# Performance work log

Hardware: AMD Instinct MI355X
Metric: run time of the kernel (lower is better)

Reference implementation:

```python
import jax, jax.numpy as jnp
import numpy as np

V = 50000        # output_size (vocab)
H = 1024         # internal hidden = hidden_size*2
L = 400          # max_length (encoder length)
B = 64
OOV_PAD = 500


def setup_inputs() -> dict:
    key = jax.random.key(0)
    ks = jax.random.split(key, 16)
    s = 0.02
    inp = {
        "input_ids": jax.random.randint(ks[0], (B,), 0, V),
        "hidden": jax.random.normal(ks[1], (1, B, H), jnp.float32),
        "encoder_outputs": jax.random.normal(ks[2], (L, B, H), jnp.float32),
        "full_input": jax.random.randint(ks[3], (B, L), 0, V),
        # parameters
        "emb": jax.random.normal(ks[4], (V, H), jnp.float32) * s,
        "attn_W": jax.random.normal(ks[5], (L, 2 * H), jnp.float32) * s,
        "attn_b": jnp.zeros((L,), jnp.float32),
        "comb_W": jax.random.normal(ks[6], (H, 2 * H), jnp.float32) * s,
        "comb_b": jnp.zeros((H,), jnp.float32),
        "W_ih": jax.random.normal(ks[7], (3 * H, H), jnp.float32) * s,
        "W_hh": jax.random.normal(ks[8], (3 * H, H), jnp.float32) * s,
        "b_ih": jnp.zeros((3 * H,), jnp.float32),
        "b_hh": jnp.zeros((3 * H,), jnp.float32),
        "out_W": jax.random.normal(ks[9], (V, H), jnp.float32) * s,
        "out_b": jnp.zeros((V,), jnp.float32),
        "gen_W": jax.random.normal(ks[10], (1, 2 * H), jnp.float32) * s,
        "gen_b": jnp.zeros((1,), jnp.float32),
    }
    return inp


def _decoder_step(input_ids, hidden, encoder_outputs, full_input,
                  emb, attn_W, attn_b, comb_W, comb_b,
                  W_ih, W_hh, b_ih, b_hh, out_W, out_b, gen_W, gen_b):
    embedded = emb[input_ids]                      # [B,H] (dropout is eval-mode identity)
    h0 = hidden[0]                                 # [B,H]

    # attention over fixed max_length positions
    cat = jnp.concatenate([embedded, h0], axis=1)  # [B,2H]
    attn_weights = jax.nn.softmax(cat @ attn_W.T + attn_b, axis=1)  # [B,L]
    enc = jnp.transpose(encoder_outputs, (1, 0, 2))                 # [B,L,H]
    attn_applied = jnp.einsum('bl,blh->bh', attn_weights, enc)      # [B,H]

    combined = jnp.concatenate([embedded, attn_applied], axis=1) @ comb_W.T + comb_b  # [B,H]

    # single-step GRU (PyTorch gate layout: r, z, n)
    gi = combined @ W_ih.T + b_ih
    gh = h0 @ W_hh.T + b_hh
    ir, iz, inn = jnp.split(gi, 3, axis=1)
    hr, hz, hn = jnp.split(gh, 3, axis=1)
    r = jax.nn.sigmoid(ir + hr)
    z = jax.nn.sigmoid(iz + hz)
    n = jnp.tanh(inn + r * hn)
    h_new = (1.0 - z) * n + z * h0                 # gru_output[0]

    p_vocab = jax.nn.log_softmax(h_new @ out_W.T + out_b, axis=1)   # [B,V]

    gen_in = jnp.concatenate([combined, h0], axis=1)                # [B,2H]
    p_gen = jax.nn.sigmoid(gen_in @ gen_W.T + gen_b)                # [B,1]

    # pointer copy distribution via scatter-add into [B, V+500]
    token_dist = jnp.zeros((input_ids.shape[0], V + OOV_PAD), p_vocab.dtype)
    rows = jnp.arange(input_ids.shape[0])[:, None]                  # [B,1]
    token_dist = token_dist.at[rows, full_input].add(attn_weights)

    p_vocab_scaled = p_vocab * p_gen
    padded = jnp.concatenate(
        [p_vocab_scaled, jnp.zeros((input_ids.shape[0], OOV_PAD), p_vocab.dtype)], axis=1)
    p_final = padded + (1.0 - p_gen) * token_dist
    # original module returns the INPUT hidden (not gru_hidden)
    return p_final, hidden, attn_weights


def reference(input_ids, hidden, encoder_outputs, full_input,
              emb, attn_W, attn_b, comb_W, comb_b,
              W_ih, W_hh, b_ih, b_hh, out_W, out_b, gen_W, gen_b):
    return _decoder_step(input_ids, hidden, encoder_outputs, full_input,
                         emb, attn_W, attn_b, comb_W, comb_b,
                         W_ih, W_hh, b_ih, b_hh, out_W, out_b, gen_W, gen_b)
```

## Files before the change

### kernel.cpp

```cpp
#include <hip/hip_runtime.h>
#include <cstddef>

#define B_ 64
#define H_ 1024
#define L_ 400
#define V_ 50000
#define VP_ 50500

typedef short short8 __attribute__((ext_vector_type(8)));
typedef float f32x4 __attribute__((ext_vector_type(4)));

static __device__ __forceinline__ short f2bf(float f) {
  unsigned u = __float_as_uint(f);
  u += 0x7fffu + ((u >> 16) & 1u);
  return (short)(u >> 16);
}

static __device__ __forceinline__ short8 pack8(float4 a, float4 b) {
  short8 r;
  r[0] = f2bf(a.x); r[1] = f2bf(a.y); r[2] = f2bf(a.z); r[3] = f2bf(a.w);
  r[4] = f2bf(b.x); r[5] = f2bf(b.y); r[6] = f2bf(b.z); r[7] = f2bf(b.w);
  return r;
}

__global__ void k_prep(const int* __restrict__ ids, const float* __restrict__ emb,
                       const float* __restrict__ hid, float* __restrict__ E,
                       float* __restrict__ A, float* __restrict__ hid_out) {
  int b = blockIdx.x;
  int t = threadIdx.x;
  int row = ids[b];
  float4 v = ((const float4*)(emb + (size_t)row * H_))[t];
  ((float4*)(E + (size_t)b * H_))[t] = v;
  ((float4*)(A + (size_t)b * H_))[t] = make_float4(0.f, 0.f, 0.f, 0.f);
  ((float4*)(hid_out + (size_t)b * H_))[t] = ((const float4*)(hid + (size_t)b * H_))[t];
}

__global__ __launch_bounds__(256) void k_gemm(
    const float* __restrict__ W, const float* __restrict__ bias,
    const float* __restrict__ X1, const float* __restrict__ X2,
    float* __restrict__ out, int N, int nkt, int ldo) {
  __shared__ short Xs[64 * 136];
  int tid = threadIdx.x;
  int wave = tid >> 6, lane = tid & 63;
  int q = lane >> 4, nl = lane & 15;
  int nbase = blockIdx.x * 64 + wave * 16 + nl;
  int nld = nbase < N ? nbase : (N - 1);
  int K = nkt * 128;
  const int ms = tid >> 2;
  const int ks0 = (tid & 3) * 32;
  f32x4 acc0 = {0.f,0.f,0.f,0.f}, acc1 = {0.f,0.f,0.f,0.f};
  f32x4 acc2 = {0.f,0.f,0.f,0.f}, acc3 = {0.f,0.f,0.f,0.f};

  for (int kt = 0; kt < nkt; ++kt) {
    const float* Xsrc = (kt < 8) ? X1 : X2;
    int kofs = (kt & 7) * 128;
    __syncthreads();
    const float4* sp = (const float4*)(Xsrc + (size_t)ms * H_ + kofs + ks0);
    #pragma unroll
    for (int i = 0; i < 4; ++i) {
      float4 f0 = sp[2 * i], f1 = sp[2 * i + 1];
      *((short8*)&Xs[ms * 136 + ks0 + i * 8]) = pack8(f0, f1);
    }
    __syncthreads();
    const float* wr = W + (size_t)nld * K + kt * 128 + q * 8;
    #pragma unroll
    for (int ks = 0; ks < 4; ++ks) {
      float4 w0 = ((const float4*)(wr + ks * 32))[0];
      float4 w1 = ((const float4*)(wr + ks * 32))[1];
      short8 bf = pack8(w0, w1);
      int ao = ks * 32 + q * 8;
      short8 a0 = *((const short8*)&Xs[(0 * 16 + nl) * 136 + ao]);
      short8 a1 = *((const short8*)&Xs[(1 * 16 + nl) * 136 + ao]);
      short8 a2 = *((const short8*)&Xs[(2 * 16 + nl) * 136 + ao]);
      short8 a3 = *((const short8*)&Xs[(3 * 16 + nl) * 136 + ao]);
      acc0 = __builtin_amdgcn_mfma_f32_16x16x32_bf16(a0, bf, acc0, 0, 0, 0);
      acc1 = __builtin_amdgcn_mfma_f32_16x16x32_bf16(a1, bf, acc1, 0, 0, 0);
      acc2 = __builtin_amdgcn_mfma_f32_16x16x32_bf16(a2, bf, acc2, 0, 0, 0);
      acc3 = __builtin_amdgcn_mfma_f32_16x16x32_bf16(a3, bf, acc3, 0, 0, 0);
    }
  }
  if (nbase < N) {
    float bv = bias[nbase];
    #pragma unroll
    for (int r = 0; r < 4; ++r) {
      int mrow = q * 4 + r;
      out[(size_t)(mrow)      * ldo + nbase] = acc0[r] + bv;
      out[(size_t)(mrow + 16) * ldo + nbase] = acc1[r] + bv;
      out[(size_t)(mrow + 32) * ldo + nbase] = acc2[r] + bv;
      out[(size_t)(mrow + 48) * ldo + nbase] = acc3[r] + bv;
    }
  }
}

__global__ void k_softmax(const float* __restrict__ S, float* __restrict__ Wout) {
  __shared__ float red[512];
  int b = blockIdx.x, t = threadIdx.x;
  float v = (t < L_) ? S[b * L_ + t] : -1e30f;
  red[t] = v; __syncthreads();
  for (int s = 256; s > 0; s >>= 1) { if (t < s) red[t] = fmaxf(red[t], red[t + s]); __syncthreads(); }
  float m = red[0]; __syncthreads();
  float e = (t < L_) ? __expf(v - m) : 0.f;
  red[t] = e; __syncthreads();
  for (int s = 256; s > 0; s >>= 1) { if (t < s) red[t] += red[t + s]; __syncthreads(); }
  float z = red[0];
  if (t < L_) Wout[b * L_ + t] = e / z;
}

__global__ void k_attnapply(const float* __restrict__ enc, const float* __restrict__ aw,
                            float* __restrict__ A) {
  int lc = blockIdx.x, b = blockIdx.y, t = threadIdx.x;
  float4 acc = make_float4(0.f, 0.f, 0.f, 0.f);
  for (int l = lc * 50; l < lc * 50 + 50; ++l) {
    float w = aw[b * L_ + l];
    float4 e = ((const float4*)(enc + ((size_t)l * B_ + b) * H_))[t];
    acc.x += w * e.x; acc.y += w * e.y; acc.z += w * e.z; acc.w += w * e.w;
  }
  float* dst = A + (size_t)b * H_ + t * 4;
  atomicAdd(dst + 0, acc.x); atomicAdd(dst + 1, acc.y);
  atomicAdd(dst + 2, acc.z); atomicAdd(dst + 3, acc.w);
}

__global__ void k_gru(const float* __restrict__ gi, const float* __restrict__ gh,
                      const float* __restrict__ hid, float* __restrict__ hnew) {
  int idx = blockIdx.x * 256 + threadIdx.x;
  int b = idx >> 10, h = idx & 1023;
  float ir = gi[b * 3072 + h], iz = gi[b * 3072 + 1024 + h], inn = gi[b * 3072 + 2048 + h];
  float hr = gh[b * 3072 + h], hz = gh[b * 3072 + 1024 + h], hn = gh[b * 3072 + 2048 + h];
  float r = 1.f / (1.f + __expf(-(ir + hr)));
  float z = 1.f / (1.f + __expf(-(iz + hz)));
  float n = tanhf(inn + r * hn);
  hnew[idx] = (1.f - z) * n + z * hid[idx];
}

__global__ void k_gen(const float* __restrict__ C, const float* __restrict__ hid,
                      const float* __restrict__ gW, const float* __restrict__ gb,
                      float* __restrict__ pg) {
  __shared__ float red[256];
  int t = threadIdx.x, b = t >> 2, p = t & 3;
  float acc = 0.f;
  for (int k = p * 512; k < p * 512 + 512; ++k) {
    float x = (k < 1024) ? C[b * H_ + k] : hid[b * H_ + k - 1024];
    acc += x * gW[k];
  }
  red[t] = acc; __syncthreads();
  if (p == 0) {
    float s = red[t] + red[t + 1] + red[t + 2] + red[t + 3] + gb[0];
    pg[b] = 1.f / (1.f + __expf(-s));
  }
}

__global__ __launch_bounds__(1024) void k_rowred(const float* __restrict__ P,
                                                 float* __restrict__ logZ) {
  __shared__ float red[1024];
  int b = blockIdx.x, t = threadIdx.x;
  float m = -1e30f;
  for (int v = t; v < V_; v += 1024) m = fmaxf(m, P[(size_t)b * VP_ + v]);
  red[t] = m; __syncthreads();
  for (int s = 512; s > 0; s >>= 1) { if (t < s) red[t] = fmaxf(red[t], red[t + s]); __syncthreads(); }
  m = red[0]; __syncthreads();
  float sum = 0.f;
  for (int v = t; v < V_; v += 1024) sum += __expf(P[(size_t)b * VP_ + v] - m);
  red[t] = sum; __syncthreads();
  for (int s = 512; s > 0; s >>= 1) { if (t < s) red[t] += red[t + s]; __syncthreads(); }
  if (t == 0) logZ[b] = m + __logf(red[0]);
}

__global__ void k_final(float* __restrict__ P, const float* __restrict__ pg,
                        const float* __restrict__ logZ) {
  int b = blockIdx.y;
  int v0 = blockIdx.x * 1024 + threadIdx.x * 4;
  if (v0 >= VP_) return;
  float g = pg[b], lz = logZ[b];
  float4* p = (float4*)(P + (size_t)b * VP_ + v0);
  if (v0 < V_) {
    float4 x = *p;
    x.x = g * (x.x - lz); x.y = g * (x.y - lz);
    x.z = g * (x.z - lz); x.w = g * (x.w - lz);
    *p = x;
  } else {
    *p = make_float4(0.f, 0.f, 0.f, 0.f);
  }
}

__global__ void k_scatter(float* __restrict__ P, const float* __restrict__ aw,
                          const int* __restrict__ fi, const float* __restrict__ pg) {
  int b = blockIdx.x, t = threadIdx.x;
  if (t >= L_) return;
  float g = 1.f - pg[b];
  int v = fi[b * L_ + t];
  atomicAdd(P + (size_t)b * VP_ + v, g * aw[b * L_ + t]);
}

extern "C" void kernel_launch(void* const* d_in, const int* in_sizes, int n_in,
                              void* d_out, int out_size, void* d_ws, size_t ws_size,
                              hipStream_t stream) {
  const int*   ids    = (const int*)d_in[0];
  const float* hid    = (const float*)d_in[1];
  const float* enc    = (const float*)d_in[2];
  const int*   fi     = (const int*)d_in[3];
  const float* emb    = (const float*)d_in[4];
  const float* attn_W = (const float*)d_in[5];
  const float* attn_b = (const float*)d_in[6];
  const float* comb_W = (const float*)d_in[7];
  const float* comb_b = (const float*)d_in[8];
  const float* W_ih   = (const float*)d_in[9];
  const float* W_hh   = (const float*)d_in[10];
  const float* b_ih   = (const float*)d_in[11];
  const float* b_hh   = (const float*)d_in[12];
  const float* out_W  = (const float*)d_in[13];
  const float* out_b  = (const float*)d_in[14];
  const float* gen_W  = (const float*)d_in[15];
  const float* gen_b  = (const float*)d_in[16];

  float* outp    = (float*)d_out;
  float* P       = outp;
  float* hid_out = outp + (size_t)B_ * VP_;
  float* aw_out  = hid_out + B_ * H_;

  float* ws = (float*)d_ws;
  float* E  = ws;
  float* A  = E + B_ * H_;
  float* C  = A + B_ * H_;
  float* HN = C + B_ * H_;
  float* S  = HN + B_ * H_;
  float* GI = S + B_ * L_;
  float* GH = GI + B_ * 3 * H_;
  float* PG = GH + B_ * 3 * H_;
  float* LZ = PG + B_;

  k_prep<<<64, 256, 0, stream>>>(ids, emb, hid, E, A, hid_out);
  k_gemm<<<7,   256, 0, stream>>>(attn_W, attn_b, E, hid, S, L_, 16, L_);
  k_softmax<<<64, 512, 0, stream>>>(S, aw_out);
  k_attnapply<<<dim3(8, 64), 256, 0, stream>>>(enc, aw_out, A);
  k_gemm<<<16,  256, 0, stream>>>(comb_W, comb_b, E, A, C, H_, 16, H_);
  k_gemm<<<48,  256, 0, stream>>>(W_ih, b_ih, C, nullptr, GI, 3 * H_, 8, 3 * H_);
  k_gemm<<<48,  256, 0, stream>>>(W_hh, b_hh, hid, nullptr, GH, 3 * H_, 8, 3 * H_);
  k_gru<<<256,  256, 0, stream>>>(GI, GH, hid, HN);
  k_gen<<<1,    256, 0, stream>>>(C, hid, gen_W, gen_b, PG);
  k_gemm<<<782, 256, 0, stream>>>(out_W, out_b, HN, nullptr, P, V_, 8, VP_);
  k_rowred<<<64, 1024, 0, stream>>>(P, LZ);
  k_final<<<dim3(50, 64), 256, 0, stream>>>(P, PG, LZ);
  k_scatter<<<64, 512, 0, stream>>>(P, aw_out, fi, PG);
}
```

Baseline: 711.4 us.

## Split-K small GEMMs, fuse softmax+attention and GRU+gen, split row reduction

Small GEMMs now use a split-K kernel that gives each wave a quarter of K and reduces through shared memory, giving more blocks and no LDS staging of X. The two GRU GEMMs run in one launch. Softmax is fused into attention-apply, GRU is fused with the p_gen dot product, and the hidden state is stored as bf16 for the vocab GEMM. The row log-sum-exp is split across four blocks per row and combined in k_final. This cuts launch count and raises parallelism on the latency-bound small stages, at the cost of redundant softmax work per block and reading X directly from global memory.

```diff
diff --git a/kernel.cpp b/kernel.cpp
--- a/kernel.cpp
+++ b/kernel.cpp
@@ -35,142 +35,195 @@
   ((float4*)(hid_out + (size_t)b * H_))[t] = ((const float4*)(hid + (size_t)b * H_))[t];
 }
 
-__global__ __launch_bounds__(256) void k_gemm(
-    const float* __restrict__ W, const float* __restrict__ bias,
-    const float* __restrict__ X1, const float* __restrict__ X2,
-    float* __restrict__ out, int N, int nkt, int ldo) {
-  __shared__ short Xs[64 * 136];
-  int tid = threadIdx.x;
-  int wave = tid >> 6, lane = tid & 63;
+__global__ __launch_bounds__(256) void k_gemm_small(
+    const float* __restrict__ W0, const float* __restrict__ bias0,
+    const float* __restrict__ Xa0, const float* __restrict__ Xb0,
+    float* __restrict__ out0, int N0, int K0, int ldo0,
+    const float* __restrict__ W1, const float* __restrict__ bias1,
+    const float* __restrict__ Xa1, const float* __restrict__ Xb1,
+    float* __restrict__ out1, int N1, int K1, int ldo1) {
+  const float* W  = blockIdx.y ? W1  : W0;
+  const float* bias = blockIdx.y ? bias1 : bias0;
+  const float* Xa = blockIdx.y ? Xa1 : Xa0;
+  const float* Xb = blockIdx.y ? Xb1 : Xb0;
+  float* out = blockIdx.y ? out1 : out0;
+  int N = blockIdx.y ? N1 : N0;
+  int K = blockIdx.y ? K1 : K0;
+  int ldo = blockIdx.y ? ldo1 : ldo0;
+
+  int tid = threadIdx.x, wave = tid >> 6, lane = tid & 63;
   int q = lane >> 4, nl = lane & 15;
-  int nbase = blockIdx.x * 64 + wave * 16 + nl;
-  int nld = nbase < N ? nbase : (N - 1);
-  int K = nkt * 128;
-  const int ms = tid >> 2;
-  const int ks0 = (tid & 3) * 32;
-  f32x4 acc0 = {0.f,0.f,0.f,0.f}, acc1 = {0.f,0.f,0.f,0.f};
-  f32x4 acc2 = {0.f,0.f,0.f,0.f}, acc3 = {0.f,0.f,0.f,0.f};
-
-  for (int kt = 0; kt < nkt; ++kt) {
-    const float* Xsrc = (kt < 8) ? X1 : X2;
-    int kofs = (kt & 7) * 128;
-    __syncthreads();
-    const float4* sp = (const float4*)(Xsrc + (size_t)ms * H_ + kofs + ks0);
+  int n = blockIdx.x * 16 + nl;
+  int nld = n < N ? n : (N - 1);
+  int kpw = K >> 2;
+  int kbeg = wave * kpw;
+  const float* wr = W + (size_t)nld * K;
+
+  f32x4 acc[4];
+  #pragma unroll
+  for (int i = 0; i < 4; ++i) acc[i] = (f32x4){0.f, 0.f, 0.f, 0.f};
+
+  for (int k0 = kbeg; k0 < kbeg + kpw; k0 += 32) {
+    int kk = k0 + q * 8;
+    float4 w0 = *(const float4*)(wr + kk);
+    float4 w1 = *(const float4*)(wr + kk + 4);
+    short8 bf = pack8(w0, w1);
+    const float* Xsel = (kk < 1024) ? Xa : Xb;
+    int kx = kk & 1023;
     #pragma unroll
-    for (int i = 0; i < 4; ++i) {
-      float4 f0 = sp[2 * i], f1 = sp[2 * i + 1];
-      *((short8*)&Xs[ms * 136 + ks0 + i * 8]) = pack8(f0, f1);
+    for (int mt = 0; mt < 4; ++mt) {
+      const float* xp = Xsel + (size_t)(mt * 16 + nl) * H_ + kx;
+      float4 x0 = *(const float4*)xp;
+      float4 x1 = *(const float4*)(xp + 4);
+      short8 af = pack8(x0, x1);
+      acc[mt] = __builtin_amdgcn_mfma_f32_16x16x32_bf16(af, bf, acc[mt], 0, 0, 0);
     }
-    __syncthreads();
-    const float* wr = W + (size_t)nld * K + kt * 128 + q * 8;
+  }
+
+  __shared__ float red[4][64][16];
+  #pragma unroll
+  for (int mt = 0; mt < 4; ++mt)
     #pragma unroll
-    for (int ks = 0; ks < 4; ++ks) {
-      float4 w0 = ((const float4*)(wr + ks * 32))[0];
-      float4 w1 = ((const float4*)(wr + ks * 32))[1];
-      short8 bf = pack8(w0, w1);
-      int ao = ks * 32 + q * 8;
-      short8 a0 = *((const short8*)&Xs[(0 * 16 + nl) * 136 + ao]);
-      short8 a1 = *((const short8*)&Xs[(1 * 16 + nl) * 136 + ao]);
-      short8 a2 = *((const short8*)&Xs[(2 * 16 + nl) * 136 + ao]);
-      short8 a3 = *((const short8*)&Xs[(3 * 16 + nl) * 136 + ao]);
-      acc0 = __builtin_amdgcn_mfma_f32_16x16x32_bf16(a0, bf, acc0, 0, 0, 0);
-      acc1 = __builtin_amdgcn_mfma_f32_16x16x32_bf16(a1, bf, acc1, 0, 0, 0);
-      acc2 = __builtin_amdgcn_mfma_f32_16x16x32_bf16(a2, bf, acc2, 0, 0, 0);
-      acc3 = __builtin_amdgcn_mfma_f32_16x16x32_bf16(a3, bf, acc3, 0, 0, 0);
+    for (int r = 0; r < 4; ++r)
+      red[wave][mt * 16 + q * 4 + r][nl] = acc[mt][r];
+  __syncthreads();
+  for (int i = tid; i < 1024; i += 256) {
+    int m = i >> 4, c = i & 15;
+    int nn = blockIdx.x * 16 + c;
+    if (nn < N) {
+      float s = red[0][m][c] + red[1][m][c] + red[2][m][c] + red[3][m][c] + bias[nn];
+      out[(size_t)m * ldo + nn] = s;
     }
   }
-  if (nbase < N) {
-    float bv = bias[nbase];
-    #pragma unroll
-    for (int r = 0; r < 4; ++r) {
-      int mrow = q * 4 + r;
-      out[(size_t)(mrow)      * ldo + nbase] = acc0[r] + bv;
-      out[(size_t)(mrow + 16) * ldo + nbase] = acc1[r] + bv;
-      out[(size_t)(mrow + 32) * ldo + nbase] = acc2[r] + bv;
-      out[(size_t)(mrow + 48) * ldo + nbase] = acc3[r] + bv;
-    }
-  }
-}
-
-__global__ void k_softmax(const float* __restrict__ S, float* __restrict__ Wout) {
-  __shared__ float red[512];
-  int b = blockIdx.x, t = threadIdx.x;
-  float v = (t < L_) ? S[b * L_ + t] : -1e30f;
-  red[t] = v; __syncthreads();
-  for (int s = 256; s > 0; s >>= 1) { if (t < s) red[t] = fmaxf(red[t], red[t + s]); __syncthreads(); }
-  float m = red[0]; __syncthreads();
-  float e = (t < L_) ? __expf(v - m) : 0.f;
-  red[t] = e; __syncthreads();
-  for (int s = 256; s > 0; s >>= 1) { if (t < s) red[t] += red[t + s]; __syncthreads(); }
+}
+
+__global__ __launch_bounds__(256) void k_attnsm(
+    const float* __restrict__ S, const float* __restrict__ enc,
+    float* __restrict__ aw_out, float* __restrict__ A) {
+  __shared__ float w[L_];
+  __shared__ float red[256];
+  int lc = blockIdx.x, b = blockIdx.y, t = threadIdx.x;
+  float a0 = S[b * L_ + t];
+  float a1 = (t < L_ - 256) ? S[b * L_ + 256 + t] : -1e30f;
+  float m = fmaxf(a0, a1);
+  red[t] = m; __syncthreads();
+  for (int s = 128; s > 0; s >>= 1) { if (t < s) red[t] = fmaxf(red[t], red[t + s]); __syncthreads(); }
+  m = red[0]; __syncthreads();
+  float e0 = __expf(a0 - m);
+  float e1 = (t < L_ - 256) ? __expf(a1 - m) : 0.f;
+  red[t] = e0 + e1; __syncthreads();
+  for (int s = 128; s > 0; s >>= 1) { if (t < s) red[t] += red[t + s]; __syncthreads(); }
   float z = red[0];
-  if (t < L_) Wout[b * L_ + t] = e / z;
-}
-
-__global__ void k_attnapply(const float* __restrict__ enc, const float* __restrict__ aw,
-                            float* __restrict__ A) {
-  int lc = blockIdx.x, b = blockIdx.y, t = threadIdx.x;
+  w[t] = e0 / z;
+  if (t < L_ - 256) w[256 + t] = e1 / z;
+  __syncthreads();
+  if (lc == 0) {
+    aw_out[b * L_ + t] = w[t];
+    if (t < L_ - 256) aw_out[b * L_ + 256 + t] = w[256 + t];
+  }
   float4 acc = make_float4(0.f, 0.f, 0.f, 0.f);
-  for (int l = lc * 50; l < lc * 50 + 50; ++l) {
-    float w = aw[b * L_ + l];
+  for (int l = lc * 25; l < lc * 25 + 25; ++l) {
+    float wg = w[l];
     float4 e = ((const float4*)(enc + ((size_t)l * B_ + b) * H_))[t];
-    acc.x += w * e.x; acc.y += w * e.y; acc.z += w * e.z; acc.w += w * e.w;
+    acc.x += wg * e.x; acc.y += wg * e.y; acc.z += wg * e.z; acc.w += wg * e.w;
   }
   float* dst = A + (size_t)b * H_ + t * 4;
   atomicAdd(dst + 0, acc.x); atomicAdd(dst + 1, acc.y);
   atomicAdd(dst + 2, acc.z); atomicAdd(dst + 3, acc.w);
 }
 
-__global__ void k_gru(const float* __restrict__ gi, const float* __restrict__ gh,
-                      const float* __restrict__ hid, float* __restrict__ hnew) {
-  int idx = blockIdx.x * 256 + threadIdx.x;
-  int b = idx >> 10, h = idx & 1023;
-  float ir = gi[b * 3072 + h], iz = gi[b * 3072 + 1024 + h], inn = gi[b * 3072 + 2048 + h];
-  float hr = gh[b * 3072 + h], hz = gh[b * 3072 + 1024 + h], hn = gh[b * 3072 + 2048 + h];
-  float r = 1.f / (1.f + __expf(-(ir + hr)));
-  float z = 1.f / (1.f + __expf(-(iz + hz)));
-  float n = tanhf(inn + r * hn);
-  hnew[idx] = (1.f - z) * n + z * hid[idx];
-}
-
-__global__ void k_gen(const float* __restrict__ C, const float* __restrict__ hid,
-                      const float* __restrict__ gW, const float* __restrict__ gb,
-                      float* __restrict__ pg) {
+__global__ __launch_bounds__(256) void k_gru_gen(
+    const float* __restrict__ gi, const float* __restrict__ gh,
+    const float* __restrict__ hid, short* __restrict__ HNb,
+    const float* __restrict__ C, const float* __restrict__ gW,
+    const float* __restrict__ gb, float* __restrict__ PG) {
   __shared__ float red[256];
-  int t = threadIdx.x, b = t >> 2, p = t & 3;
-  float acc = 0.f;
-  for (int k = p * 512; k < p * 512 + 512; ++k) {
-    float x = (k < 1024) ? C[b * H_ + k] : hid[b * H_ + k - 1024];
-    acc += x * gW[k];
-  }
-  red[t] = acc; __syncthreads();
-  if (p == 0) {
-    float s = red[t] + red[t + 1] + red[t + 2] + red[t + 3] + gb[0];
-    pg[b] = 1.f / (1.f + __expf(-s));
-  }
-}
-
-__global__ __launch_bounds__(1024) void k_rowred(const float* __restrict__ P,
-                                                 float* __restrict__ logZ) {
-  __shared__ float red[1024];
-  int b = blockIdx.x, t = threadIdx.x;
+  int blk = blockIdx.x, t = threadIdx.x;
+  if (blk < 256) {
+    int idx = blk * 256 + t;
+    int b = idx >> 10, h = idx & 1023;
+    float ir = gi[b * 3072 + h], iz = gi[b * 3072 + 1024 + h], inn = gi[b * 3072 + 2048 + h];
+    float hr = gh[b * 3072 + h], hz = gh[b * 3072 + 1024 + h], hn = gh[b * 3072 + 2048 + h];
+    float r = 1.f / (1.f + __expf(-(ir + hr)));
+    float z = 1.f / (1.f + __expf(-(iz + hz)));
+    float n = tanhf(inn + r * hn);
+    HNb[idx] = f2bf((1.f - z) * n + z * hid[idx]);
+  } else {
+    int b = blk - 256;
+    float acc = 0.f;
+    for (int k = t; k < 2 * H_; k += 256) {
+      float x = (k < H_) ? C[b * H_ + k] : hid[b * H_ + k - H_];
+      acc += x * gW[k];
+    }
+    red[t] = acc; __syncthreads();
+    for (int s = 128; s > 0; s >>= 1) { if (t < s) red[t] += red[t + s]; __syncthreads(); }
+    if (t == 0) PG[b] = 1.f / (1.f + __expf(-(red[0] + gb[0])));
+  }
+}
+
+__global__ __launch_bounds__(256) void k_gemm_vocab(
+    const short* __restrict__ Xb, const float* __restrict__ W,
+    const float* __restrict__ bias, float* __restrict__ P) {
+  int tid = threadIdx.x, wave = tid >> 6, lane = tid & 63;
+  int q = lane >> 4, nl = lane & 15;
+  int n = blockIdx.x * 64 + wave * 16 + nl;
+  int nld = n < V_ ? n : (V_ - 1);
+  const float* wr = W + (size_t)nld * H_;
+  f32x4 acc[4];
+  #pragma unroll
+  for (int i = 0; i < 4; ++i) acc[i] = (f32x4){0.f, 0.f, 0.f, 0.f};
+
+  for (int k0 = 0; k0 < H_; k0 += 32) {
+    int kk = k0 + q * 8;
+    float4 w0 = *(const float4*)(wr + kk);
+    float4 w1 = *(const float4*)(wr + kk + 4);
+    short8 bf = pack8(w0, w1);
+    #pragma unroll
+    for (int mt = 0; mt < 4; ++mt) {
+      short8 af = *(const short8*)(Xb + (size_t)(mt * 16 + nl) * H_ + kk);
+      acc[mt] = __builtin_amdgcn_mfma_f32_16x16x32_bf16(af, bf, acc[mt], 0, 0, 0);
+    }
+  }
+  if (n < V_) {
+    float bv = bias[n];
+    #pragma unroll
+    for (int mt = 0; mt < 4; ++mt)
+      #pragma unroll
+      for (int r = 0; r < 4; ++r)
+        P[(size_t)(mt * 16 + q * 4 + r) * VP_ + n] = acc[mt][r] + bv;
+  }
+}
+
+__global__ __launch_bounds__(256) void k_rowred2(const float* __restrict__ P,
+                                                 float* __restrict__ MX,
+                                                 float* __restrict__ SE) {
+  __shared__ float red[256];
+  int b = blockIdx.x >> 2, c = blockIdx.x & 3;
+  int t = threadIdx.x;
+  int v0 = c * 12500, v1 = v0 + 12500;
   float m = -1e30f;
-  for (int v = t; v < V_; v += 1024) m = fmaxf(m, P[(size_t)b * VP_ + v]);
+  for (int v = v0 + t; v < v1; v += 256) m = fmaxf(m, P[(size_t)b * VP_ + v]);
   red[t] = m; __syncthreads();
-  for (int s = 512; s > 0; s >>= 1) { if (t < s) red[t] = fmaxf(red[t], red[t + s]); __syncthreads(); }
+  for (int s = 128; s > 0; s >>= 1) { if (t < s) red[t] = fmaxf(red[t], red[t + s]); __syncthreads(); }
   m = red[0]; __syncthreads();
   float sum = 0.f;
-  for (int v = t; v < V_; v += 1024) sum += __expf(P[(size_t)b * VP_ + v] - m);
+  for (int v = v0 + t; v < v1; v += 256) sum += __expf(P[(size_t)b * VP_ + v] - m);
   red[t] = sum; __syncthreads();
-  for (int s = 512; s > 0; s >>= 1) { if (t < s) red[t] += red[t + s]; __syncthreads(); }
-  if (t == 0) logZ[b] = m + __logf(red[0]);
+  for (int s = 128; s > 0; s >>= 1) { if (t < s) red[t] += red[t + s]; __syncthreads(); }
+  if (t == 0) { MX[blockIdx.x] = m; SE[blockIdx.x] = red[0]; }
 }
 
 __global__ void k_final(float* __restrict__ P, const float* __restrict__ pg,
-                        const float* __restrict__ logZ) {
+                        const float* __restrict__ MX, const float* __restrict__ SE) {
   int b = blockIdx.y;
+  float m0 = MX[b * 4], m1 = MX[b * 4 + 1], m2 = MX[b * 4 + 2], m3 = MX[b * 4 + 3];
+  float M = fmaxf(fmaxf(m0, m1), fmaxf(m2, m3));
+  float Z = SE[b * 4] * __expf(m0 - M) + SE[b * 4 + 1] * __expf(m1 - M)
+          + SE[b * 4 + 2] * __expf(m2 - M) + SE[b * 4 + 3] * __expf(m3 - M);
+  float lz = M + __logf(Z);
+  float g = pg[b];
   int v0 = blockIdx.x * 1024 + threadIdx.x * 4;
   if (v0 >= VP_) return;
-  float g = pg[b], lz = logZ[b];
   float4* p = (float4*)(P + (size_t)b * VP_ + v0);
   if (v0 < V_) {
     float4 x = *p;
@@ -218,27 +271,31 @@
   float* aw_out  = hid_out + B_ * H_;
 
   float* ws = (float*)d_ws;
-  float* E  = ws;
-  float* A  = E + B_ * H_;
-  float* C  = A + B_ * H_;
-  float* HN = C + B_ * H_;
-  float* S  = HN + B_ * H_;
-  float* GI = S + B_ * L_;
-  float* GH = GI + B_ * 3 * H_;
-  float* PG = GH + B_ * 3 * H_;
-  float* LZ = PG + B_;
+  float* E   = ws;
+  float* A   = E + B_ * H_;
+  float* C   = A + B_ * H_;
+  float* S   = C + B_ * H_;
+  float* GI  = S + B_ * L_;
+  float* GH  = GI + B_ * 3 * H_;
+  float* PG  = GH + B_ * 3 * H_;
+  float* MX  = PG + B_;
+  float* SE  = MX + 256;
+  short* HNb = (short*)(SE + 256);
 
   k_prep<<<64, 256, 0, stream>>>(ids, emb, hid, E, A, hid_out);
-  k_gemm<<<7,   256, 0, stream>>>(attn_W, attn_b, E, hid, S, L_, 16, L_);
-  k_softmax<<<64, 512, 0, stream>>>(S, aw_out);
-  k_attnapply<<<dim3(8, 64), 256, 0, stream>>>(enc, aw_out, A);
-  k_gemm<<<16,  256, 0, stream>>>(comb_W, comb_b, E, A, C, H_, 16, H_);
-  k_gemm<<<48,  256, 0, stream>>>(W_ih, b_ih, C, nullptr, GI, 3 * H_, 8, 3 * H_);
-  k_gemm<<<48,  256, 0, stream>>>(W_hh, b_hh, hid, nullptr, GH, 3 * H_, 8, 3 * H_);
-  k_gru<<<256,  256, 0, stream>>>(GI, GH, hid, HN);
-  k_gen<<<1,    256, 0, stream>>>(C, hid, gen_W, gen_b, PG);
-  k_gemm<<<782, 256, 0, stream>>>(out_W, out_b, HN, nullptr, P, V_, 8, VP_);
-  k_rowred<<<64, 1024, 0, stream>>>(P, LZ);
-  k_final<<<dim3(50, 64), 256, 0, stream>>>(P, PG, LZ);
+  k_gemm_small<<<dim3(25, 1), 256, 0, stream>>>(
+      attn_W, attn_b, E, hid, S, L_, 2 * H_, L_,
+      attn_W, attn_b, E, hid, S, L_, 2 * H_, L_);
+  k_attnsm<<<dim3(16, 64), 256, 0, stream>>>(S, enc, aw_out, A);
+  k_gemm_small<<<dim3(64, 1), 256, 0, stream>>>(
+      comb_W, comb_b, E, A, C, H_, 2 * H_, H_,
+      comb_W, comb_b, E, A, C, H_, 2 * H_, H_);
+  k_gemm_small<<<dim3(192, 2), 256, 0, stream>>>(
+      W_ih, b_ih, C, C, GI, 3 * H_, H_, 3 * H_,
+      W_hh, b_hh, hid, hid, GH, 3 * H_, H_, 3 * H_);
+  k_gru_gen<<<320, 256, 0, stream>>>(GI, GH, hid, HNb, C, gen_W, gen_b, PG);
+  k_gemm_vocab<<<782, 256, 0, stream>>>(HNb, out_W, out_b, P);
+  k_rowred2<<<256, 256, 0, stream>>>(P, MX, SE);
+  k_final<<<dim3(50, 64), 256, 0, stream>>>(P, PG, MX, SE);
   k_scatter<<<64, 512, 0, stream>>>(P, aw_out, fi, PG);
 }
```

Measured after the change: 609.9 us. 14.3% less time.
